# Performance work log

Hardware: AMD Instinct MI355X
Metric: run time of the kernel (lower is better)

## Reference

```python
import jax, jax.numpy as jnp
import numpy as np

D_MODEL, N_HEADS, D_FF = 1024, 16, 4096
SCALE = 0.1          # lookup-activation input quantization step
NUM_BITS = 8
LEVELS = 1 << NUM_BITS   # 256
HALF = LEVELS // 2       # 128
MAX_EXP = 4
EPS = 1e-5


def pow2_weight(key, shape, max_exp=MAX_EXP):
    """Ternary power-of-two weights: values in {0, +/-2^{-e}}, e in [max_exp, max_exp+3].
    Exponent range keeps fan-in-1024 outputs O(1)."""
    k1, k2 = jax.random.split(key)
    sign = jax.random.randint(k1, shape, -1, 2).astype(jnp.float32)  # {-1,0,1}
    e = jax.random.randint(k2, shape, max_exp, max_exp + 4).astype(jnp.float32)
    return sign * jnp.exp2(-e)


def setup_inputs() -> dict:
    key = jax.random.key(0)
    ks = jax.random.split(key, 8)
    x = jax.random.normal(ks[0], (4, 2048, D_MODEL), dtype=jnp.float32)
    return {
        "x": x,
        "ln1_g": jnp.ones((D_MODEL,), jnp.float32),
        "ln1_b": jnp.zeros((D_MODEL,), jnp.float32),
        "wq": pow2_weight(ks[1], (D_MODEL, D_MODEL)),
        "wk": pow2_weight(ks[2], (D_MODEL, D_MODEL)),
        "wv": pow2_weight(ks[3], (D_MODEL, D_MODEL)),
        "wo": pow2_weight(ks[4], (D_MODEL, D_MODEL)),
        "ln2_g": jnp.ones((D_MODEL,), jnp.float32),
        "ln2_b": jnp.zeros((D_MODEL,), jnp.float32),
        "w1": pow2_weight(ks[5], (D_MODEL, D_FF)),
        "w2": pow2_weight(ks[6], (D_FF, D_MODEL)),
    }


def _layernorm(x, g, b):
    mu = jnp.mean(x, axis=-1, keepdims=True)
    var = jnp.var(x, axis=-1, keepdims=True)
    return (x - mu) * jax.lax.rsqrt(var + EPS) * g + b


def _lookup_act(x):
    # StructuredLookupActivation: quantize input to 2^num_bits levels, gather from
    # a precomputed GELU table (proved via Lasso lookup in the SNARK).
    grid = (jnp.arange(LEVELS, dtype=jnp.float32) - HALF) * SCALE
    table = jax.nn.gelu(grid)
    idx = jnp.clip(jnp.round(x / SCALE).astype(jnp.int32) + HALF, 0, LEVELS - 1)
    return table[idx]


def _linear_attention(x, wq, wk, wv, wo):
    B, S, D = x.shape
    H, Dh = N_HEADS, D // N_HEADS
    q = (x @ wq).reshape(B, S, H, Dh)
    k = (x @ wk).reshape(B, S, H, Dh)
    v = (x @ wv).reshape(B, S, H, Dh)
    # elu+1 feature map -> O(S*Dh^2) linear attention (no [S,S] scores)
    phi_q = jax.nn.elu(q) + 1.0
    phi_k = jax.nn.elu(k) + 1.0
    kv = jnp.einsum('bshd,bshe->bhde', phi_k, v)          # [B,H,Dh,Dh]
    z = jnp.sum(phi_k, axis=1)                            # [B,H,Dh]
    num = jnp.einsum('bshd,bhde->bshe', phi_q, kv)        # [B,S,H,Dh]
    den = jnp.einsum('bshd,bhd->bsh', phi_q, z)[..., None] + 1e-6
    out = (num / den).reshape(B, S, D)
    return out @ wo


def reference(x, ln1_g, ln1_b, wq, wk, wv, wo, ln2_g, ln2_b, w1, w2):
    # norm -> linear attention -> residual
    x = x + _linear_attention(_layernorm(x, ln1_g, ln1_b), wq, wk, wv, wo)
    # norm -> ternary FFN with lookup activation -> residual
    h = _layernorm(x, ln2_g, ln2_b)
    x = x + (_lookup_act(h @ w1) @ w2)
    return x
```

## Files before the change

kernel.cpp:

```cpp
#include <hip/hip_runtime.h>
#include <cstdint>
#include <cstddef>


#define D_MODEL 1024
#define SEQ     2048
#define BATCH   4
#define NTOK    8192
#define NHEADS  16
#define DH      64
#define DFF     4096
#define KVCH    16
#define CHROWS  (SEQ / KVCH)
#define PSTRIDE 4160

typedef _Float16 half8 __attribute__((ext_vector_type(8)));
typedef float f32x4 __attribute__((ext_vector_type(4)));

__device__ __forceinline__ unsigned short f2h(float x) {
  _Float16 h = (_Float16)x;
  union { _Float16 h; unsigned short u; } c; c.h = h; return c.u;
}

__device__ __forceinline__ float phi_act(float x) {
  return x > 0.f ? x + 1.f : expf(x);
}

__device__ __forceinline__ float gelu_lut(float x) {
  float r = rintf(x / 0.1f);
  r = fminf(fmaxf(r, -128.f), 127.f);
  float v = r * 0.1f;
  float c = 0.7978845608028654f;
  float t = tanhf(c * (v + 0.044715f * v * v * v));
  return 0.5f * v * (1.f + t);
}

__device__ __forceinline__ void gl_lds16(const void* g, void* l) {
  __builtin_amdgcn_global_load_lds(
      (const __attribute__((address_space(1))) unsigned int*)g,
      (__attribute__((address_space(3))) unsigned int*)l, 16, 0, 0);
}

__global__ __launch_bounds__(256) void convT(const float* __restrict__ W,
                                             unsigned short* __restrict__ WT,
                                             int K, int N) {
  __shared__ float tile[64][65];
  int kb = blockIdx.y << 6, nb = blockIdx.x << 6;
  int t = threadIdx.x;
  int rr = t >> 4, cc = (t & 15) << 2;
#pragma unroll
  for (int i = 0; i < 4; ++i) {
    int r = rr + (i << 4);
    float4 v = *(const float4*)(W + (size_t)(kb + r) * N + nb + cc);
    tile[r][cc] = v.x; tile[r][cc + 1] = v.y; tile[r][cc + 2] = v.z; tile[r][cc + 3] = v.w;
  }
  __syncthreads();
#pragma unroll
  for (int i = 0; i < 4; ++i) {
    int n = rr + (i << 4);
    ushort4 o;
    o.x = f2h(tile[cc + 0][n]); o.y = f2h(tile[cc + 1][n]);
    o.z = f2h(tile[cc + 2][n]); o.w = f2h(tile[cc + 3][n]);
    *(ushort4*)(WT + (size_t)(nb + n) * K + kb + cc) = o;
  }
}

__global__ __launch_bounds__(256) void ln_kernel(const float* __restrict__ X,
                                                 const float* __restrict__ g,
                                                 const float* __restrict__ b,
                                                 unsigned short* __restrict__ Y) {
  int tok = blockIdx.x;
  int t = threadIdx.x;
  const float4* xr = (const float4*)(X + (size_t)tok * D_MODEL);
  float4 v = xr[t];
  float s  = v.x + v.y + v.z + v.w;
  float s2 = v.x * v.x + v.y * v.y + v.z * v.z + v.w * v.w;
#pragma unroll
  for (int o = 32; o > 0; o >>= 1) {
    s  += __shfl_down(s, o);
    s2 += __shfl_down(s2, o);
  }
  __shared__ float red[8];
  __shared__ float mu_s, rs_s;
  int wid = t >> 6;
  if ((t & 63) == 0) { red[wid] = s; red[wid + 4] = s2; }
  __syncthreads();
  if (t == 0) {
    float ts  = red[0] + red[1] + red[2] + red[3];
    float ts2 = red[4] + red[5] + red[6] + red[7];
    float mu  = ts * (1.f / D_MODEL);
    float var = ts2 * (1.f / D_MODEL) - mu * mu;
    mu_s = mu;
    rs_s = rsqrtf(var + 1e-5f);
  }
  __syncthreads();
  float mu = mu_s, rs = rs_s;
  float4 gv = ((const float4*)g)[t];
  float4 bv = ((const float4*)b)[t];
  ushort4 hv;
  hv.x = f2h((v.x - mu) * rs * gv.x + bv.x);
  hv.y = f2h((v.y - mu) * rs * gv.y + bv.y);
  hv.z = f2h((v.z - mu) * rs * gv.z + bv.z);
  hv.w = f2h((v.w - mu) * rs * gv.w + bv.w);
  ((ushort4*)(Y + (size_t)tok * D_MODEL))[t] = hv;
}

template <int EP>
__global__ __launch_bounds__(256, 2) void mfma_gemm(
    const unsigned short* __restrict__ A,
    const unsigned short* __restrict__ BT,
    void* Cv, const float* R, int N, int K) {
  __shared__ unsigned short smem[2 * 8192];
  unsigned short* sA = smem;
  unsigned short* sB = smem + 8192;

  int t = threadIdx.x;
  int w = t >> 6, l = t & 63;
  int rl = l >> 3, cl = l & 7;
  int gseg = (cl ^ rl) << 4;
  int m0 = blockIdx.y << 7;
  int n0 = blockIdx.x << 7;
  size_t strideB = (size_t)K * 2;

  const char* gA[4]; const char* gB[4];
  int ldsOff[4];
  for (int j = 0; j < 4; ++j) {
    int row = (w << 5) + (j << 3) + rl;
    gA[j] = (const char*)A + (size_t)(m0 + row) * strideB + gseg;
    gB[j] = (const char*)BT + (size_t)(n0 + row) * strideB + gseg;
    ldsOff[j] = ((w << 5) + (j << 3)) << 6;
  }

  int wm = w >> 1, wn = w & 1;
  int m16 = l & 15, qd = l >> 4;

  f32x4 acc[4][4];
#pragma unroll
  for (int i = 0; i < 4; ++i)
#pragma unroll
    for (int j = 0; j < 4; ++j) acc[i][j] = (f32x4){0.f, 0.f, 0.f, 0.f};

  for (int k0 = 0; k0 < K; k0 += 64) {
    size_t kb = (size_t)k0 * 2;
#pragma unroll
    for (int j = 0; j < 4; ++j) {
      gl_lds16(gA[j] + kb, sA + ldsOff[j]);
      gl_lds16(gB[j] + kb, sB + ldsOff[j]);
    }
    __syncthreads();
#pragma unroll
    for (int kk = 0; kk < 2; ++kk) {
      int ksb = (kk << 2) + qd;
      half8 af[4], bf[4];
#pragma unroll
      for (int mt = 0; mt < 4; ++mt) {
        int r = (wm << 6) + (mt << 4) + m16;
        int slot = ksb ^ (r & 7);
        af[mt] = *(const half8*)(sA + (r << 6) + (slot << 3));
      }
#pragma unroll
      for (int nt = 0; nt < 4; ++nt) {
        int r = (wn << 6) + (nt << 4) + m16;
        int slot = ksb ^ (r & 7);
        bf[nt] = *(const half8*)(sB + (r << 6) + (slot << 3));
      }
#pragma unroll
      for (int mt = 0; mt < 4; ++mt)
#pragma unroll
        for (int nt = 0; nt < 4; ++nt)
          acc[mt][nt] = __builtin_amdgcn_mfma_f32_16x16x32_f16(af[mt], bf[nt], acc[mt][nt], 0, 0, 0);
    }
    __syncthreads();
  }

  int colBase = n0 + (wn << 6) + m16;
#pragma unroll
  for (int mt = 0; mt < 4; ++mt) {
    int rBase = m0 + (wm << 6) + (mt << 4) + (qd << 2);
#pragma unroll
    for (int nt = 0; nt < 4; ++nt) {
      int col = colBase + (nt << 4);
#pragma unroll
      for (int i = 0; i < 4; ++i) {
        size_t idx = (size_t)(rBase + i) * N + col;
        float v = acc[mt][nt][i];
        if (EP == 1)      ((float*)Cv)[idx] = phi_act(v);
        else if (EP == 2) ((float*)Cv)[idx] = R[idx] + v;
        else if (EP == 3) ((unsigned short*)Cv)[idx] = f2h(gelu_lut(v));
        else              ((float*)Cv)[idx] = v;
      }
    }
  }
}

__global__ __launch_bounds__(256) void kvz_partial(const float* __restrict__ PK,
                                                   const float* __restrict__ V,
                                                   float* __restrict__ P) {
  int c = blockIdx.x, bh = blockIdx.y;
  int b = bh >> 4, h = bh & 15;
  __shared__ float pk[8][64];
  __shared__ float vv[8][64];
  int t = threadIdx.x;
  const size_t base = ((size_t)b * SEQ + (size_t)c * CHROWS) * D_MODEL + h * DH;
  int u = t & 127;
  int lrow = u >> 4;
  int lcol = (u & 15) << 2;
  bool isV = (t >= 128);
  const float* src = isV ? V : PK;
  int dkb = (t >> 4) << 2;
  int deb = (t & 15) << 2;
  float acc[4][4] = {};
  float zacc = 0.f;
  for (int s0 = 0; s0 < CHROWS; s0 += 8) {
    float4 ld = *(const float4*)(src + base + (size_t)(s0 + lrow) * D_MODEL + lcol);
    __syncthreads();
    if (isV) *(float4*)&vv[lrow][lcol] = ld;
    else     *(float4*)&pk[lrow][lcol] = ld;
    __syncthreads();
#pragma unroll
    for (int ss = 0; ss < 8; ++ss) {
      float4 a  = *(const float4*)&pk[ss][dkb];
      float4 bb = *(const float4*)&vv[ss][deb];
      acc[0][0] += a.x * bb.x; acc[0][1] += a.x * bb.y; acc[0][2] += a.x * bb.z; acc[0][3] += a.x * bb.w;
      acc[1][0] += a.y * bb.x; acc[1][1] += a.y * bb.y; acc[1][2] += a.y * bb.z; acc[1][3] += a.y * bb.w;
      acc[2][0] += a.z * bb.x; acc[2][1] += a.z * bb.y; acc[2][2] += a.z * bb.z; acc[2][3] += a.z * bb.w;
      acc[3][0] += a.w * bb.x; acc[3][1] += a.w * bb.y; acc[3][2] += a.w * bb.z; acc[3][3] += a.w * bb.w;
    }
    if (t < 64) {
#pragma unroll
      for (int ss = 0; ss < 8; ++ss) zacc += pk[ss][t];
    }
  }
  float* Pb = P + ((size_t)c * 64 + bh) * PSTRIDE;
#pragma unroll
  for (int i = 0; i < 4; ++i) {
    float4 o; o.x = acc[i][0]; o.y = acc[i][1]; o.z = acc[i][2]; o.w = acc[i][3];
    *(float4*)(Pb + (size_t)(dkb + i) * DH + deb) = o;
  }
  if (t < 64) Pb[4096 + t] = zacc;
}

__global__ __launch_bounds__(256) void kvz_reduce(const float* __restrict__ P,
                                                  float* __restrict__ KV,
                                                  float* __restrict__ Z) {
  int bh = blockIdx.x;
  int t = threadIdx.x;
  for (int i = t; i < PSTRIDE; i += 256) {
    float s = 0.f;
#pragma unroll
    for (int c = 0; c < KVCH; ++c)
      s += P[((size_t)c * 64 + bh) * PSTRIDE + i];
    if (i < 4096) KV[(size_t)bh * 4096 + i] = s;
    else          Z[(size_t)bh * 64 + (i - 4096)] = s;
  }
}

__global__ __launch_bounds__(256) void attn_kernel(const float* __restrict__ PQ,
                                                   const float* __restrict__ KVm,
                                                   const float* __restrict__ Z,
                                                   unsigned short* __restrict__ O) {
  int s0 = blockIdx.x << 6;
  int h = blockIdx.y, b = blockIdx.z;
  __shared__ float Pqt[64][64];
  __shared__ float Kv[64][64];
  __shared__ float den[64];
  __shared__ float zsh[64];
  int t = threadIdx.x;
  size_t qbase  = ((size_t)b * SEQ + s0) * D_MODEL + h * DH;
  size_t kvbase = (size_t)(b * NHEADS + h) * (DH * DH);
  int r0 = t >> 4;
  int c4 = (t & 15) << 2;
#pragma unroll
  for (int rr = 0; rr < 4; ++rr) {
    int row = r0 + (rr << 4);
    *(float4*)&Kv[row][c4] = *(const float4*)(KVm + kvbase + (size_t)row * DH + c4);
    float4 q = *(const float4*)(PQ + qbase + (size_t)row * D_MODEL + c4);
    Pqt[c4 + 0][row] = q.x;
    Pqt[c4 + 1][row] = q.y;
    Pqt[c4 + 2][row] = q.z;
    Pqt[c4 + 3][row] = q.w;
  }
  if (t < 16) *(float4*)&zsh[t << 2] = *(const float4*)(Z + (size_t)(b * NHEADS + h) * DH + (t << 2));
  __syncthreads();
  if (t < 64) {
    float d_ = 1e-6f;
#pragma unroll
    for (int dd = 0; dd < 64; ++dd) d_ += Pqt[dd][t] * zsh[dd];
    den[t] = d_;
  }
  __syncthreads();
  int tokb = (t >> 4) << 2, eb = (t & 15) << 2;
  float acc[4][4] = {};
#pragma unroll 8
  for (int dd = 0; dd < 64; ++dd) {
    float4 a  = *(const float4*)&Pqt[dd][tokb];
    float4 bb = *(const float4*)&Kv[dd][eb];
    acc[0][0] += a.x * bb.x; acc[0][1] += a.x * bb.y; acc[0][2] += a.x * bb.z; acc[0][3] += a.x * bb.w;
    acc[1][0] += a.y * bb.x; acc[1][1] += a.y * bb.y; acc[1][2] += a.y * bb.z; acc[1][3] += a.y * bb.w;
    acc[2][0] += a.z * bb.x; acc[2][1] += a.z * bb.y; acc[2][2] += a.z * bb.z; acc[2][3] += a.z * bb.w;
    acc[3][0] += a.w * bb.x; acc[3][1] += a.w * bb.y; acc[3][2] += a.w * bb.z; acc[3][3] += a.w * bb.w;
  }
#pragma unroll
  for (int i = 0; i < 4; ++i) {
    float dv = den[tokb + i];
    ushort4 hv;
    hv.x = f2h(acc[i][0] / dv);
    hv.y = f2h(acc[i][1] / dv);
    hv.z = f2h(acc[i][2] / dv);
    hv.w = f2h(acc[i][3] / dv);
    size_t oidx = ((size_t)b * SEQ + s0 + tokb + i) * D_MODEL + h * DH + eb;
    *(ushort4*)(O + oidx) = hv;
  }
}

extern "C" void kernel_launch(void* const* d_in, const int* in_sizes, int n_in,
                              void* d_out, int out_size, void* d_ws, size_t ws_size,
                              hipStream_t stream) {
  const float* x    = (const float*)d_in[0];
  const float* ln1g = (const float*)d_in[1];
  const float* ln1b = (const float*)d_in[2];
  const float* wq   = (const float*)d_in[3];
  const float* wk   = (const float*)d_in[4];
  const float* wv   = (const float*)d_in[5];
  const float* wo   = (const float*)d_in[6];
  const float* ln2g = (const float*)d_in[7];
  const float* ln2b = (const float*)d_in[8];
  const float* w1   = (const float*)d_in[9];
  const float* w2   = (const float*)d_in[10];
  float* out = (float*)d_out;
  char* ws = (char*)d_ws;

  const size_t MB = 1024 * 1024;
  unsigned short* xn   = (unsigned short*)(ws);
  float*          phiq = (float*)(ws + 32 * MB);
  float*          phik = (float*)(ws + 64 * MB);
  float*          vbuf = (float*)(ws + 96 * MB);
  unsigned short* ffn  = (unsigned short*)(ws + 32 * MB);
  unsigned short* w1T  = (unsigned short*)(ws + 96 * MB);
  unsigned short* w2T  = (unsigned short*)(ws + 104 * MB);
  unsigned short* woT  = (unsigned short*)(ws + 128 * MB);

  unsigned short* wqT = (unsigned short*)d_out;
  unsigned short* wkT = wqT + (size_t)D_MODEL * D_MODEL;
  unsigned short* wvT = wkT + (size_t)D_MODEL * D_MODEL;
  float* kvP = (float*)((char*)d_out + 6 * MB);
  float* kv  = (float*)((char*)d_out + 24 * MB);
  float* z   = (float*)((char*)d_out + 25 * MB);

  dim3 blk(256);
  dim3 gcD(D_MODEL / 64, D_MODEL / 64);

  convT<<<gcD, blk, 0, stream>>>(wq, wqT, D_MODEL, D_MODEL);
  convT<<<gcD, blk, 0, stream>>>(wk, wkT, D_MODEL, D_MODEL);
  convT<<<gcD, blk, 0, stream>>>(wv, wvT, D_MODEL, D_MODEL);
  convT<<<gcD, blk, 0, stream>>>(wo, woT, D_MODEL, D_MODEL);

  ln_kernel<<<NTOK, blk, 0, stream>>>(x, ln1g, ln1b, xn);

  dim3 gD(D_MODEL / 128, NTOK / 128);
  mfma_gemm<1><<<gD, blk, 0, stream>>>(xn, wqT, phiq, nullptr, D_MODEL, D_MODEL);
  mfma_gemm<1><<<gD, blk, 0, stream>>>(xn, wkT, phik, nullptr, D_MODEL, D_MODEL);
  mfma_gemm<0><<<gD, blk, 0, stream>>>(xn, wvT, vbuf, nullptr, D_MODEL, D_MODEL);

  kvz_partial<<<dim3(KVCH, BATCH * NHEADS), blk, 0, stream>>>(phik, vbuf, kvP);
  kvz_reduce<<<BATCH * NHEADS, blk, 0, stream>>>(kvP, kv, z);

  attn_kernel<<<dim3(SEQ / 64, NHEADS, BATCH), blk, 0, stream>>>(phiq, kv, z, xn);

  convT<<<dim3(DFF / 64, D_MODEL / 64), blk, 0, stream>>>(w1, w1T, D_MODEL, DFF);
  convT<<<dim3(D_MODEL / 64, DFF / 64), blk, 0, stream>>>(w2, w2T, DFF, D_MODEL);

  mfma_gemm<2><<<gD, blk, 0, stream>>>(xn, woT, out, x, D_MODEL, D_MODEL);

  ln_kernel<<<NTOK, blk, 0, stream>>>(out, ln2g, ln2b, xn);

  dim3 gF(DFF / 128, NTOK / 128);
  mfma_gemm<3><<<gF, blk, 0, stream>>>(xn, w1T, ffn, nullptr, DFF, D_MODEL);

  mfma_gemm<2><<<gD, blk, 0, stream>>>(ffn, w2T, out, out, D_MODEL, DFF);
}
```

Measured before the change: 510.7 us.

## Add LDS GELU table, XCD-aware block swizzle, raise GEMM occupancy

The FFN1 epilogue now reads GELU values from a 256-entry shared-memory table filled at kernel start, replacing a per-element tanh evaluation. Block indices are remapped so that consecutive M-tiles stay on the same XCD, which is meant to improve L2 reuse of the A and B tiles. Launch bounds rise from 2 to 4 blocks per SM, which restricts register use and could cause spills in the 4x4 accumulator loop. No barrier separates the table fill from the epilogue reads, but the main loop's syncthreads already orders them.

```diff
diff --git a/kernel.cpp b/kernel.cpp
--- a/kernel.cpp
+++ b/kernel.cpp
@@ -26,10 +26,7 @@
   return x > 0.f ? x + 1.f : expf(x);
 }
 
-__device__ __forceinline__ float gelu_lut(float x) {
-  float r = rintf(x / 0.1f);
-  r = fminf(fmaxf(r, -128.f), 127.f);
-  float v = r * 0.1f;
+__device__ __forceinline__ float gelu_exact(float v) {
   float c = 0.7978845608028654f;
   float t = tanhf(c * (v + 0.044715f * v * v * v));
   return 0.5f * v * (1.f + t);
@@ -106,20 +103,36 @@
 }
 
 template <int EP>
-__global__ __launch_bounds__(256, 2) void mfma_gemm(
+__global__ __launch_bounds__(256, 4) void mfma_gemm(
     const unsigned short* __restrict__ A,
     const unsigned short* __restrict__ BT,
     void* Cv, const float* R, int N, int K) {
   __shared__ unsigned short smem[2 * 8192];
+  __shared__ float gtab[EP == 3 ? 256 : 1];
   unsigned short* sA = smem;
   unsigned short* sB = smem + 8192;
 
   int t = threadIdx.x;
+  if (EP == 3) gtab[t & 255] = gelu_exact((float)((t & 255) - 128) * 0.1f);
+
+  int bm, bn;
+  {
+    int L = blockIdx.y * gridDim.x + blockIdx.x;
+    if ((gridDim.y & 7) == 0) {
+      int xcd = L & 7, wi = L >> 3;
+      int mPerX = gridDim.y >> 3;
+      bm = xcd * mPerX + wi / gridDim.x;
+      bn = wi % gridDim.x;
+    } else {
+      bn = blockIdx.x; bm = blockIdx.y;
+    }
+  }
+
   int w = t >> 6, l = t & 63;
   int rl = l >> 3, cl = l & 7;
   int gseg = (cl ^ rl) << 4;
-  int m0 = blockIdx.y << 7;
-  int n0 = blockIdx.x << 7;
+  int m0 = bm << 7;
+  int n0 = bn << 7;
   size_t strideB = (size_t)K * 2;
 
   const char* gA[4]; const char* gB[4];
@@ -186,8 +199,12 @@
         float v = acc[mt][nt][i];
         if (EP == 1)      ((float*)Cv)[idx] = phi_act(v);
         else if (EP == 2) ((float*)Cv)[idx] = R[idx] + v;
-        else if (EP == 3) ((unsigned short*)Cv)[idx] = f2h(gelu_lut(v));
-        else              ((float*)Cv)[idx] = v;
+        else if (EP == 3) {
+          float r = rintf(v / 0.1f);
+          int iq = (int)r + 128;
+          iq = iq < 0 ? 0 : (iq > 255 ? 255 : iq);
+          ((unsigned short*)Cv)[idx] = f2h(gtab[iq]);
+        } else            ((float*)Cv)[idx] = v;
       }
     }
   }
```

Result: faster. 496.9 us (-2.7%).
